# Performance work log

Hardware: AMD Instinct MI355X
Metric: run time of the kernel (lower is better)

Reference implementation:

```python
import jax, jax.numpy as jnp
from jax import lax
import numpy as np

K = 32        # self.k: neighbors queried per center
TOP = 5       # inner topk size (hardcoded in source)
MAX_ITER = 16 # bound on the data-dependent while loop; leftovers emitted at final iter


def _refine_one(pc, centers, ids):
    """Vectorized translation of the per-batch while-loop.

    Instead of shrinking the sample set each iteration (data-dependent shape),
    every sample is tracked with an `active` flag and a convergence-iteration
    stamp. Emitting order in the torch code is (iteration, surviving-order),
    and boolean masking preserves relative original order, so a stable sort by
    (conv_iter, original_index) reproduces the exact concatenation order.
    """
    N, D = pc.shape
    S = centers.shape[0]
    ar = jnp.arange(S)

    def knn(q):  # q: [S,3] -> [S,K] indices of nearest cloud points (ascending dist)
        d2 = jnp.sum((q[:, None, :] - pc[None, :, :]) ** 2, axis=-1)  # [S,N]
        _, ind = lax.top_k(-d2, K)
        return ind

    def step(cur_pts, cur_idx):
        ind = knn(cur_pts)                                   # [S,K]
        nbh = pc[ind]                                        # [S,K,3]
        gc = jnp.mean(nbh, axis=1)                           # [S,3]
        dist = jnp.linalg.norm(nbh - gc[:, None, :], axis=2) # [S,K]
        _, top = lax.top_k(-dist, TOP)                       # [S,TOP] smallest dists
        in_top = jnp.any(top == 0, axis=1)                   # center (col 0) stable?
        new_idx = ind[ar, top[:, 0]]                         # point closest to centroid
        return ind, in_top, new_idx

    def body(it, st):
        cur_pts, cur_idx, conv_it, out_pts, out_idx, out_grp, active = st
        ind, in_top, new_idx = step(cur_pts, cur_idx)
        newly = active & in_top
        conv_it = jnp.where(newly, it, conv_it)
        out_pts = jnp.where(newly[:, None], cur_pts, out_pts)
        out_idx = jnp.where(newly, cur_idx, out_idx)
        out_grp = jnp.where(newly[:, None], ind, out_grp)
        move = active & ~in_top
        cur_idx = jnp.where(move, new_idx, cur_idx)
        cur_pts = jnp.where(move[:, None], pc[new_idx], cur_pts)
        return (cur_pts, cur_idx, conv_it, out_pts, out_idx, out_grp, move)

    st0 = (centers, ids,
           jnp.full((S,), MAX_ITER, jnp.int32),
           jnp.zeros((S, D), pc.dtype),
           jnp.zeros((S,), ids.dtype),
           jnp.zeros((S, K), jnp.int32),
           jnp.ones((S,), bool))
    cur_pts, cur_idx, conv_it, out_pts, out_idx, out_grp, active = lax.fori_loop(
        0, MAX_ITER, body, st0)

    # force-emit any sample that never converged within MAX_ITER
    ind, _, _ = step(cur_pts, cur_idx)
    out_pts = jnp.where(active[:, None], cur_pts, out_pts)
    out_idx = jnp.where(active, cur_idx, out_idx)
    out_grp = jnp.where(active[:, None], ind, out_grp)

    order = jnp.argsort(conv_it * (S + 1) + ar)  # stable (iter, orig-pos) order
    return out_pts[order], out_idx[order], out_grp[order]


def setup_inputs() -> dict:
    key = jax.random.key(0)
    k1, k2, k3 = jax.random.split(key, 3)
    B, N, S = 8, 8192, 1024
    xyz = jax.random.normal(k1, (B, N, 3), jnp.float32)
    center = jax.random.normal(k2, (B, S, 3), jnp.float32)
    idx = jax.random.randint(k3, (B, S), 0, N, jnp.int32)
    return {"xyz": xyz, "center": center, "idx": idx}


def reference(xyz, center, idx):
    assert xyz.shape[0] == center.shape[0]
    C, I1, I2 = jax.vmap(_refine_one)(xyz, center, idx)
    # torch runs under no_grad; outputs are detached constants
    return (lax.stop_gradient(C), I1, I2)
```

## Files before the change

### kernel.cpp

```cpp
#include <hip/hip_runtime.h>
#include <stdint.h>

#define BATCH   8
#define NPTS    8192
#define SCH     1024
#define KNN     32
#define TOPC    5
#define MAXIT   16
#define NCELL   4096
#define NGRP    128
#define NSEED   6
#define FCAP    128

typedef unsigned long long ull;
typedef float vf2 __attribute__((ext_vector_type(2)));
typedef float vf4 __attribute__((ext_vector_type(4)));

#define SENTKEY ((((ull)0x7F800000u) << 13) | 0x1FFFull)

#define ROTL(lane, g) (((lane) + (g) * 17) & 63)

__device__ __forceinline__ uint32_t xshfl32(uint32_t v, int xl) {
    if (xl == 1)
        return (uint32_t)__builtin_amdgcn_update_dpp((int)v, (int)v, 0xB1, 0xF, 0xF, true);
    if (xl == 2)
        return (uint32_t)__builtin_amdgcn_update_dpp((int)v, (int)v, 0x4E, 0xF, 0xF, true);
    return (uint32_t)__shfl_xor((int)v, xl, 64);
}
__device__ __forceinline__ ull xshfl64(ull v, int xl) {
    uint32_t lo = xshfl32((uint32_t)v, xl);
    uint32_t hi = xshfl32((uint32_t)(v >> 32), xl);
    return ((ull)hi << 32) | lo;
}
__device__ __forceinline__ float xshflf(float v, int xl) {
    return __uint_as_float(xshfl32(__float_as_uint(v), xl));
}

__device__ __forceinline__ float d2_exact(vf4 q, vf4 p) {
#pragma clang fp contract(off)
    vf2 d = q.xy - p.xy;
    vf2 s = d * d;
    float dz = q.z - p.z;
    float sz = dz * dz;
    return (s.x + s.y) + sz;
}

__device__ __forceinline__ void insert_top4(ull key, ull& k0, ull& k1, ull& k2,
                                            ull& k3, float& th) {
    if (key < k3) {
        k3 = key;
        { bool c = k3 < k2; ull mn = c ? k3 : k2, mx = c ? k2 : k3; k2 = mn; k3 = mx; }
        { bool c = k2 < k1; ull mn = c ? k2 : k1, mx = c ? k1 : k2; k1 = mn; k2 = mx; }
        { bool c = k1 < k0; ull mn = c ? k1 : k0, mx = c ? k0 : k1; k0 = mn; k1 = mx; }
        th = __uint_as_float((uint32_t)(k3 >> 13));
    }
}

__device__ __forceinline__ ull wave_min_u64(ull k) {
#pragma unroll
    for (int off = 32; off; off >>= 1) {
        ull o = xshfl64(k, off);
        k = o < k ? o : k;
    }
    return k;
}
__device__ __forceinline__ ull wave_max_u64(ull k) {
#pragma unroll
    for (int off = 32; off; off >>= 1) {
        ull o = xshfl64(k, off);
        k = o > k ? o : k;
    }
    return k;
}

__device__ __forceinline__ float bbox_mind2(vf4 q, vf4 c, vf4 h) {
    float dx = fmaxf(fabsf(q.x - c.x) - h.x, 0.f);
    float dy = fmaxf(fabsf(q.y - c.y) - h.y, 0.f);
    float dz = fmaxf(fabsf(q.z - c.z) - h.z, 0.f);
    return (dx * dx + dy * dy + dz * dz) * 0.9999f;
}

__device__ __forceinline__ ull cx(ull v, int xl, bool keepmin) {
    ull o = xshfl64(v, xl);
    return ((v < o) == keepmin) ? v : o;
}
__device__ __forceinline__ void cswap(ull& a, ull& b, bool up) {
    bool lt = a < b;
    ull mn = lt ? a : b, mx = lt ? b : a;
    a = up ? mn : mx;
    b = up ? mx : mn;
}

__device__ __forceinline__ uint32_t cx32(uint32_t v, int xl, bool keepmin) {
    uint32_t o = xshfl32(v, xl);
    return ((v < o) == keepmin) ? v : o;
}
__device__ __forceinline__ void cswap32(uint32_t& a, uint32_t& b, bool up) {
    uint32_t mn = a < b ? a : b, mx = a < b ? b : a;
    a = up ? mn : mx;
    b = up ? mx : mn;
}

__device__ __forceinline__ void sort128_u32(uint32_t& s0, uint32_t& s1, int lane) {
    cswap32(s0, s1, true);
    if (lane & 1) { uint32_t t = s0; s0 = s1; s1 = t; }
#pragma unroll
    for (int kk = 4; kk <= 128; kk <<= 1) {
        const bool up = (lane & (kk >> 1)) == 0;
#pragma unroll
        for (int d = kk >> 1; d >= 2; d >>= 1) {
            const int xl = d >> 1;
            const bool keepmin = (up == ((lane & xl) == 0));
            s0 = cx32(s0, xl, keepmin);
            s1 = cx32(s1, xl, keepmin);
        }
        cswap32(s0, s1, up);
    }
}

__device__ __forceinline__ void sort128_u64(ull& s0, ull& s1, int lane) {
    cswap(s0, s1, true);
    if (lane & 1) { ull t = s0; s0 = s1; s1 = t; }
#pragma unroll
    for (int kk = 4; kk <= 128; kk <<= 1) {
        const bool up = (lane & (kk >> 1)) == 0;
#pragma unroll
        for (int d = kk >> 1; d >= 2; d >>= 1) {
            const int xl = d >> 1;
            const bool keepmin = (up == ((lane & xl) == 0));
            s0 = cx(s0, xl, keepmin);
            s1 = cx(s1, xl, keepmin);
        }
        cswap(s0, s1, up);
    }
}

__device__ __forceinline__ int next_gid(ull& r0, ull& r1) {
    if (r0) { int g = __ffsll((unsigned long long)r0) - 1; r0 &= r0 - 1; return g; }
    if (r1) { int g = __ffsll((unsigned long long)r1) - 1; r1 &= r1 - 1; return 64 + g; }
    return -1;
}

__device__ __forceinline__ int cell_of(float x, float y, float z) {
    int cxi = min(15, max(0, (int)floorf((x + 4.0f) * 2.0f)));
    int cyi = min(15, max(0, (int)floorf((y + 4.0f) * 2.0f)));
    int czi = min(15, max(0, (int)floorf((z + 4.0f) * 2.0f)));
    uint32_t sx = (cxi & 1) | ((cxi & 2) << 2) | ((cxi & 4) << 4) | ((cxi & 8) << 6);
    uint32_t sy = (cyi & 1) | ((cyi & 2) << 2) | ((cyi & 4) << 4) | ((cyi & 8) << 6);
    uint32_t sz = (czi & 1) | ((czi & 2) << 2) | ((czi & 4) << 4) | ((czi & 8) << 6);
    return (int)(sx | (sy << 1) | (sz << 2));
}

__device__ __attribute__((noinline)) int serial_topk_masked(
    const vf4* __restrict__ Psort, vf4 q, int lane, ull sm0, ull sm1) {
    ull k0 = SENTKEY, k1 = SENTKEY, k2 = SENTKEY, k3 = SENTKEY;
    int s0 = 0, s1 = 0, s2 = 0, s3 = 0;
    float th = __builtin_inff();
    for (int gid = 0; gid < NGRP; ++gid) {
        bool sel = (gid < 64) ? ((sm0 >> gid) & 1ull) : ((sm1 >> (gid - 64)) & 1ull);
        if (!sel) continue;
        vf4 p = Psort[(gid << 6) + lane];
        float d2 = d2_exact(q, p);
        uint32_t oi = __float_as_uint(p.w);
        ull key = ((ull)__float_as_uint(d2) << 13) | oi;
        if (d2 <= th && key < k3) {
            k3 = key; s3 = gid;
            if (k3 < k2) { ull t = k2; k2 = k3; k3 = t; int ts = s2; s2 = s3; s3 = ts; }
            if (k2 < k1) { ull t = k1; k1 = k2; k2 = t; int ts = s1; s1 = s2; s2 = ts; }
            if (k1 < k0) { ull t = k0; k0 = k1; k1 = t; int ts = s0; s0 = s1; s1 = ts; }
            th = __uint_as_float((uint32_t)(k3 >> 13));
        }
    }
    ull em0 = 0ull, em1 = 0ull;
    int cnt = 4, my_ind = 0;
    for (int r = 0; r < KNN; ++r) {
        ull gmin = wave_min_u64(k0);
        int widx = (int)(gmin & 0x1FFFull);
        if (lane == r) my_ind = widx;
        if (k0 == gmin) {
            int g = s0;
            if (g < 64) em0 |= 1ull << g; else em1 |= 1ull << (g - 64);
            k0 = k1; k1 = k2; k2 = k3; k3 = SENTKEY;
            s0 = s1; s1 = s2; s2 = s3;
            if (--cnt == 0) {
                k0 = k1 = k2 = k3 = SENTKEY;
                float th2 = __builtin_inff();
                for (int gid = 0; gid < NGRP; ++gid) {
                    bool sel = (gid < 64) ? ((sm0 >> gid) & 1ull)
                                          : ((sm1 >> (gid - 64)) & 1ull);
                    bool ex = (gid < 64) ? ((em0 >> gid) & 1ull)
                                         : ((em1 >> (gid - 64)) & 1ull);
                    if (!sel || ex) continue;
                    vf4 p = Psort[(gid << 6) + lane];
                    float d2 = d2_exact(q, p);
                    uint32_t oi = __float_as_uint(p.w);
                    ull key = ((ull)__float_as_uint(d2) << 13) | oi;
                    if (d2 <= th2 && key < k3) {
                        k3 = key; s3 = gid;
                        if (k3 < k2) { ull t = k2; k2 = k3; k3 = t; int ts = s2; s2 = s3; s3 = ts; }
                        if (k2 < k1) { ull t = k1; k1 = k2; k2 = t; int ts = s1; s1 = s2; s2 = ts; }
                        if (k1 < k0) { ull t = k0; k0 = k1; k1 = t; int ts = s0; s0 = s1; s1 = ts; }
                        th2 = __uint_as_float((uint32_t)(k3 >> 13));
                    }
                }
                cnt = 4;
            }
        }
    }
    return my_ind;
}

__device__ int collect_topk(const vf4* __restrict__ Psort, vf4 q, int lane,
                            ull sm0, ull sm1, ull tau,
                            ull* buf, int* cnt) {
    if (lane == 0) *cnt = 0;
    __asm__ volatile("s_waitcnt lgkmcnt(0)" ::: "memory");
    ull r0 = sm0, r1 = sm1;
    int g = next_gid(r0, r1);
    while (g >= 0) {
        vf4 p = Psort[(g << 6) + lane];
        float d2 = d2_exact(q, p);
        ull key = ((ull)__float_as_uint(d2) << 13) | __float_as_uint(p.w);
        if (key <= tau) {
            int pos = atomicAdd(cnt, 1);
            if (pos < FCAP) buf[pos] = key;
        }
        g = next_gid(r0, r1);
    }
    __asm__ volatile("s_waitcnt lgkmcnt(0)" ::: "memory");
    const int M = *cnt;
    if (M > FCAP) return -1;
    ull s0 = (2 * lane + 0 < M) ? buf[2 * lane + 0] : SENTKEY;
    ull s1 = (2 * lane + 1 < M) ? buf[2 * lane + 1] : SENTKEY;
    sort128_u64(s0, s1, lane);
    const int src = lane >> 1;
    const uint32_t e0 = (uint32_t)__shfl((int)(uint32_t)s0, src, 64);
    const uint32_t e1 = (uint32_t)__shfl((int)(uint32_t)s1, src, 64);
    return (int)(((lane & 1) ? e1 : e0) & 0x1FFFu);
}

__global__ __launch_bounds__(256) void prep_kernel(const float* __restrict__ xyz,
                                                   vf4* __restrict__ pc4,
                                                   int* __restrict__ counts) {
    int i = (int)(blockIdx.x * blockDim.x + threadIdx.x);
    if (i >= BATCH * NPTS) return;
    vf4 v;
    v.x = xyz[(size_t)i * 3 + 0];
    v.y = xyz[(size_t)i * 3 + 1];
    v.z = xyz[(size_t)i * 3 + 2];
    v.w = 0.f;
    pc4[i] = v;
    int b = i >> 13;
    atomicAdd(&counts[b * NCELL + cell_of(v.x, v.y, v.z)], 1);
}

__global__ __launch_bounds__(1024) void scan_kernel(const int* __restrict__ counts,
                                                    int* __restrict__ cursor) {
    int b = (int)blockIdx.x, tid = (int)threadIdx.x;
    int lane = tid & 63, w = tid >> 6;
    __shared__ int wsum[16];
    int base = b * NCELL + tid * 4;
    int v0 = counts[base], v1 = counts[base + 1], v2 = counts[base + 2], v3 = counts[base + 3];
    int s = v0 + v1 + v2 + v3;
    int incl = s;
#pragma unroll
    for (int off = 1; off < 64; off <<= 1) {
        int o = __shfl_up(incl, off, 64);
        if (lane >= off) incl += o;
    }
    if (lane == 63) wsum[w] = incl;
    __syncthreads();
    if (tid == 0) {
        int acc = 0;
#pragma unroll
        for (int i = 0; i < 16; ++i) { int x = wsum[i]; wsum[i] = acc; acc += x; }
    }
    __syncthreads();
    int excl = incl - s + wsum[w];
    cursor[base]     = excl;
    cursor[base + 1] = excl + v0;
    cursor[base + 2] = excl + v0 + v1;
    cursor[base + 3] = excl + v0 + v1 + v2;
}

__global__ __launch_bounds__(256) void scatter_kernel(const vf4* __restrict__ pc4,
                                                      int* __restrict__ cursor,
                                                      vf4* __restrict__ sortedP) {
    int i = (int)(blockIdx.x * blockDim.x + threadIdx.x);
    if (i >= BATCH * NPTS) return;
    vf4 v = pc4[i];
    int b = i >> 13, pi = i & (NPTS - 1);
    int c = cell_of(v.x, v.y, v.z);
    int pos = atomicAdd(&cursor[b * NCELL + c], 1);
    v.w = __uint_as_float((uint32_t)pi);
    sortedP[((size_t)b << 13) + pos] = v;
}

__global__ __launch_bounds__(256) void bbox_kernel(const vf4* __restrict__ sortedP,
                                                   vf4* __restrict__ bC,
                                                   vf4* __restrict__ bH) {
    int g = (int)((blockIdx.x * blockDim.x + threadIdx.x) >> 6);
    int lane = (int)(threadIdx.x & 63);
    vf4 p = sortedP[((size_t)g << 6) + lane];
    float mnx = p.x, mxx = p.x, mny = p.y, mxy = p.y, mnz = p.z, mxz = p.z;
#pragma unroll
    for (int off = 32; off; off >>= 1) {
        mnx = fminf(mnx, xshflf(mnx, off));
        mxx = fmaxf(mxx, xshflf(mxx, off));
        mny = fminf(mny, xshflf(mny, off));
        mxy = fmaxf(mxy, xshflf(mxy, off));
        mnz = fminf(mnz, xshflf(mnz, off));
        mxz = fmaxf(mxz, xshflf(mxz, off));
    }
    if (lane == 0) {
        vf4 c, h;
        c.x = (mnx + mxx) * 0.5f; c.y = (mny + mxy) * 0.5f; c.z = (mnz + mxz) * 0.5f; c.w = 0.f;
        h.x = (mxx - mnx) * 0.5f; h.y = (mxy - mny) * 0.5f; h.z = (mxz - mnz) * 0.5f; h.w = 0.f;
        bC[g] = c;
        bH[g] = h;
    }
}

__global__ __launch_bounds__(256)
__attribute__((amdgpu_waves_per_eu(2, 4)))
void refine_kernel(
    const vf4* __restrict__ pc4, const vf4* __restrict__ sortedP,
    const vf4* __restrict__ bC, const vf4* __restrict__ bH,
    const float* __restrict__ center, const int* __restrict__ idx_in,
    float* __restrict__ pts_ws, int* __restrict__ idx_ws,
    int* __restrict__ grp_ws, int* __restrict__ conv_ws) {
    const int lane = (int)(threadIdx.x & 63);
    const int w = (int)(threadIdx.x >> 6);
    const int b = (int)(blockIdx.x & 7);
    const int s = (((int)blockIdx.x >> 3) << 2) + w;
    const vf4* __restrict__ Porig = pc4 + ((size_t)b << 13);
    const vf4* __restrict__ Psort = sortedP + ((size_t)b << 13);

    __shared__ vf4 sbC[NGRP], sbH[NGRP];
    __shared__ vf4 nbh[4][KNN];
    __shared__ ull fbuf[4][FCAP];
    __shared__ int fcnt[4];

    {
        const int t = (int)threadIdx.x;
        if (t < NGRP) sbC[t] = bC[(b << 7) + t];
        else          sbH[t - NGRP] = bH[(b << 7) + (t - NGRP)];
    }
    __syncthreads();

    const size_t ch = ((size_t)b << 10) + (size_t)s;
    vf4 q;
    q.x = center[ch * 3 + 0];
    q.y = center[ch * 3 + 1];
    q.z = center[ch * 3 + 2];
    q.w = 0.f;
    int qidx = idx_in[ch];

    int conv = MAXIT;
    int my_ind = 0;
    vf4 myp = q;
    bool warm = false;

    for (int it = 0;; ++it) {
        const vf4 c0 = sbC[lane],      h0 = sbH[lane];
        const vf4 c1 = sbC[64 + lane], h1 = sbH[64 + lane];
        const float m0 = bbox_mind2(q, c0, h0);
        const float m1 = bbox_mind2(q, c1, h1);

        ull k0 = SENTKEY, k1 = SENTKEY, k2 = SENTKEY, k3 = SENTKEY;
        float th = __builtin_inff();
        ull sm0 = 0ull, sm1 = 0ull, am0 = 0ull, am1 = 0ull;
        float th0 = __builtin_inff();

        bool fastwarm = false;
        if (warm) {
            const float dw = (lane < KNN) ? d2_exact(q, myp) : 0.f;
            th0 = dw;
#pragma unroll
            for (int off = 32; off; off >>= 1)
                th0 = fmaxf(th0, xshflf(th0, off));
            sm0 = __ballot(m0 <= th0);
            sm1 = __ballot(m1 <= th0);
            const int nsel = __popcll(sm0) + __popcll(sm1);
            if (nsel <= 20) { fastwarm = true; am0 = sm0; am1 = sm1; }
        }

        if (!fastwarm) {
            sm0 = 0ull; sm1 = 0ull;
            uint32_t g0k = ((__float_as_uint(m0) >> 6) << 7) | (uint32_t)lane;
            uint32_t g1k = ((__float_as_uint(m1) >> 6) << 7) | (uint32_t)(64 + lane);
            sort128_u32(g0k, g1k, lane);
#pragma unroll
            for (int r = 0; r < NSEED; ++r) {
                const uint32_t nk = (r & 1)
                    ? (uint32_t)__shfl((int)g1k, r >> 1, 64)
                    : (uint32_t)__shfl((int)g0k, r >> 1, 64);
                const int gid = (int)(nk & 127u);
                if (gid < 64) sm0 |= 1ull << gid; else sm1 |= 1ull << (gid - 64);
                const vf4 p = Psort[(gid << 6) + ROTL(lane, gid)];
                const float d2 = d2_exact(q, p);
                if (d2 <= th)
                    insert_top4(((ull)__float_as_uint(d2) << 13) | __float_as_uint(p.w),
                                k0, k1, k2, k3, th);
            }
            ull t = k0;
            {
                ull o = xshfl64(t, 32);
                t = o < t ? o : t;
            }
            const ull B = wave_max_u64(t);
            const float Bd = fminf(__uint_as_float((uint32_t)(B >> 13)), th0);
            am0 = __ballot(m0 <= Bd) & ~sm0;
            am1 = __ballot(m1 <= Bd) & ~sm1;
            sm0 |= am0; sm1 |= am1;
        }

        {
            ull rem0 = am0, rem1 = am1;
            int ga = next_gid(rem0, rem1);
            while (ga >= 0) {
                const int gb2 = next_gid(rem0, rem1);
                const vf4 pa = Psort[(ga << 6) + ROTL(lane, ga)];
                vf4 pb;
                if (gb2 >= 0) pb = Psort[(gb2 << 6) + ROTL(lane, gb2)];
                const float da = d2_exact(q, pa);
                if (da <= th)
                    insert_top4(((ull)__float_as_uint(da) << 13) | __float_as_uint(pa.w),
                                k0, k1, k2, k3, th);
                if (gb2 >= 0) {
                    const float dbv = d2_exact(q, pb);
                    if (dbv <= th)
                        insert_top4(((ull)__float_as_uint(dbv) << 13) | __float_as_uint(pb.w),
                                    k0, k1, k2, k3, th);
                }
                ga = next_gid(rem0, rem1);
            }
        }
        const ull prek3 = k3;

        const bool odd = (lane & 1) != 0;
        ull a0 = odd ? k3 : k0;
        ull a1 = odd ? k2 : k1;
        ull a2 = odd ? k1 : k2;
        ull a3 = odd ? k0 : k3;
#pragma unroll
        for (int kk = 8; kk <= 256; kk <<= 1) {
            const bool up = (lane & (kk >> 2)) == 0;
#pragma unroll
            for (int d = kk >> 1; d >= 4; d >>= 1) {
                const int xl = d >> 2;
                const bool keepmin = (up == ((lane & xl) == 0));
                a0 = cx(a0, xl, keepmin);
                a1 = cx(a1, xl, keepmin);
                a2 = cx(a2, xl, keepmin);
                a3 = cx(a3, xl, keepmin);
            }
            cswap(a0, a2, up); cswap(a1, a3, up);
            cswap(a0, a1, up); cswap(a2, a3, up);
        }
        const ull tau = (ull)__shfl((unsigned long long)a3, 7, 64);
        const ull bad = __ballot(prek3 < tau);
        if (bad != 0ull) {
            const int mi = collect_topk(Psort, q, lane, sm0, sm1, tau,
                                        fbuf[w], &fcnt[w]);
            my_ind = (mi >= 0) ? mi : serial_topk_masked(Psort, q, lane, sm0, sm1);
        } else {
            const int src = lane >> 2;
            const uint32_t lo0 = (uint32_t)__shfl((int)(uint32_t)a0, src, 64);
            const uint32_t lo1 = (uint32_t)__shfl((int)(uint32_t)a1, src, 64);
            const uint32_t lo2 = (uint32_t)__shfl((int)(uint32_t)a2, src, 64);
            const uint32_t lo3 = (uint32_t)__shfl((int)(uint32_t)a3, src, 64);
            const int sel = lane & 3;
            uint32_t lo = (sel == 0) ? lo0 : (sel == 1) ? lo1 : (sel == 2) ? lo2 : lo3;
            my_ind = (int)(lo & 0x1FFFu);
        }

        if (it == MAXIT) break;

        myp = q;
        if (lane < KNN) {
            myp = Porig[my_ind];
            nbh[w][lane] = myp;
        }
        __asm__ volatile("s_waitcnt lgkmcnt(0)" ::: "memory");
        float sx = 0.f, sy = 0.f, sz = 0.f;
#pragma unroll
        for (int j = 0; j < KNN; ++j) {
            vf4 pj = nbh[w][j];
            sx = __fadd_rn(sx, pj.x);
            sy = __fadd_rn(sy, pj.y);
            sz = __fadd_rn(sz, pj.z);
        }
        const float gx = __fmul_rn(sx, 0.03125f);
        const float gy = __fmul_rn(sy, 0.03125f);
        const float gz = __fmul_rn(sz, 0.03125f);

        float dj = __builtin_inff();
        if (lane < KNN) {
            const float dx = __fsub_rn(myp.x, gx);
            const float dy = __fsub_rn(myp.y, gy);
            const float dz = __fsub_rn(myp.z, gz);
            dj = sqrtf(__fadd_rn(__fadd_rn(__fmul_rn(dx, dx), __fmul_rn(dy, dy)),
                                 __fmul_rn(dz, dz)));
        }
        const uint32_t db = __float_as_uint(dj);
        const uint32_t d0 = (uint32_t)__shfl((int)db, 0, 64);
        const ull bal = __ballot(db < d0);
        if (__popcll(bal) <= TOPC - 1) { conv = it; break; }

        uint32_t m = db;
#pragma unroll
        for (int off = 32; off; off >>= 1) {
            uint32_t o = xshfl32(m, off);
            m = o < m ? o : m;
        }
        const ull balm = __ballot(db == m);
        const int jm = __ffsll((unsigned long long)balm) - 1;
        qidx = __shfl(my_ind, jm, 64);
        q.x = __shfl(myp.x, jm, 64);
        q.y = __shfl(myp.y, jm, 64);
        q.z = __shfl(myp.z, jm, 64);
        q.w = 0.f;
        warm = true;
    }

    if (lane < KNN) grp_ws[ch * KNN + lane] = my_ind;
    if (lane == 0) {
        pts_ws[ch * 3 + 0] = q.x;
        pts_ws[ch * 3 + 1] = q.y;
        pts_ws[ch * 3 + 2] = q.z;
        idx_ws[ch] = qidx;
        conv_ws[ch] = conv;
    }
}

__global__ __launch_bounds__(1024) void order_kernel(
    const float* __restrict__ pts_ws, const int* __restrict__ idx_ws,
    const int* __restrict__ grp_ws, const int* __restrict__ conv_ws,
    float* __restrict__ out) {
    const int b = (int)blockIdx.x;
    const int s = (int)threadIdx.x;
    const int w = s >> 6, l = s & 63;
    __shared__ int wavecnt[16][MAXIT + 1];
    __shared__ int binbase[MAXIT + 1];
    const size_t ch = (size_t)b * SCH + s;
    const int c = conv_ws[ch];
    int rw = 0;
#pragma unroll
    for (int v = 0; v <= MAXIT; ++v) {
        ull bal = __ballot(c == v);
        if (l == 0) wavecnt[w][v] = (int)__popcll(bal);
        if (c == v) rw = (int)__popcll(bal & ((1ull << l) - 1ull));
    }
    __syncthreads();
    if (s == 0) {
        int acc = 0;
        for (int v = 0; v <= MAXIT; ++v) {
            int t = 0;
            for (int w2 = 0; w2 < 16; ++w2) t += wavecnt[w2][v];
            binbase[v] = acc;
            acc += t;
        }
    }
    __syncthreads();
    int pos = binbase[c] + rw;
    for (int w2 = 0; w2 < w; ++w2) pos += wavecnt[w2][c];

    float* __restrict__ C  = out;
    float* __restrict__ I1 = out + (size_t)BATCH * SCH * 3;
    float* __restrict__ I2 = I1 + (size_t)BATCH * SCH;
    const size_t o = (size_t)b * SCH + pos;
    C[o * 3 + 0] = pts_ws[ch * 3 + 0];
    C[o * 3 + 1] = pts_ws[ch * 3 + 1];
    C[o * 3 + 2] = pts_ws[ch * 3 + 2];
    I1[o] = (float)idx_ws[ch];
#pragma unroll
    for (int k = 0; k < KNN; ++k) I2[o * KNN + k] = (float)grp_ws[ch * KNN + k];
}

extern "C" void kernel_launch(void* const* d_in, const int* in_sizes, int n_in,
                              void* d_out, int out_size, void* d_ws, size_t ws_size,
                              hipStream_t stream) {
    const float* xyz    = (const float*)d_in[0];
    const float* center = (const float*)d_in[1];
    const int*   idx_in = (const int*)d_in[2];
    float* out = (float*)d_out;

    char* wp = (char*)d_ws;
    vf4* pc4     = (vf4*)wp;  wp += (size_t)BATCH * NPTS * sizeof(vf4);
    vf4* sortedP = (vf4*)wp;  wp += (size_t)BATCH * NPTS * sizeof(vf4);
    vf4* bC      = (vf4*)wp;  wp += (size_t)BATCH * NGRP * sizeof(vf4);
    vf4* bH      = (vf4*)wp;  wp += (size_t)BATCH * NGRP * sizeof(vf4);
    int* counts  = (int*)wp;  wp += (size_t)BATCH * NCELL * 4;
    int* cursor  = (int*)wp;  wp += (size_t)BATCH * NCELL * 4;
    float* pts_ws = (float*)wp; wp += (size_t)BATCH * SCH * 3 * 4;
    int*   idx_ws = (int*)wp;   wp += (size_t)BATCH * SCH * 4;
    int*   grp_ws = (int*)wp;   wp += (size_t)BATCH * SCH * KNN * 4;
    int*   conv_ws = (int*)wp;

    hipMemsetAsync(counts, 0, (size_t)BATCH * NCELL * 4, stream);
    prep_kernel<<<(BATCH * NPTS + 255) / 256, 256, 0, stream>>>(xyz, pc4, counts);
    scan_kernel<<<BATCH, 1024, 0, stream>>>(counts, cursor);
    scatter_kernel<<<(BATCH * NPTS + 255) / 256, 256, 0, stream>>>(pc4, cursor, sortedP);
    bbox_kernel<<<(BATCH * NGRP * 64) / 256, 256, 0, stream>>>(sortedP, bC, bH);

    const int chains = BATCH * SCH;
    refine_kernel<<<chains * 64 / 256, 256, 0, stream>>>(
        pc4, sortedP, bC, bH, center, idx_in, pts_ws, idx_ws, grp_ws, conv_ws);
    order_kernel<<<BATCH, SCH, 0, stream>>>(pts_ws, idx_ws, grp_ws, conv_ws, out);
}
```

Baseline: 180.8 us.

## Fuse bbox computation into scatter via atomics and ordering into refine tail

Removes the separate bbox kernel by computing per-group min/max bounds with order-preserving float-encoded atomicMin/Max inside the scatter kernel. Also removes the order kernel: the last refine block per batch, found through an atomic done counter, computes the convergence-order permutation with shared bitmasks and writes the outputs. This saves two launches but adds many contended global atomics in scatter and serialises the ordering work onto a single tail block per batch with 256 threads.

```diff
diff --git a/kernel.cpp b/kernel.cpp
--- a/kernel.cpp
+++ b/kernel.cpp
@@ -20,6 +20,15 @@
 
 #define ROTL(lane, g) (((lane) + (g) * 17) & 63)
 
+__device__ __forceinline__ uint32_t fenc(float f) {
+    uint32_t b = __float_as_uint(f);
+    return (b & 0x80000000u) ? ~b : (b | 0x80000000u);
+}
+__device__ __forceinline__ float fdec(uint32_t u) {
+    uint32_t b = (u & 0x80000000u) ? (u & 0x7FFFFFFFu) : ~u;
+    return __uint_as_float(b);
+}
+
 __device__ __forceinline__ uint32_t xshfl32(uint32_t v, int xl) {
     if (xl == 1)
         return (uint32_t)__builtin_amdgcn_update_dpp((int)v, (int)v, 0xB1, 0xF, 0xF, true);
@@ -73,10 +82,10 @@
     return k;
 }
 
-__device__ __forceinline__ float bbox_mind2(vf4 q, vf4 c, vf4 h) {
-    float dx = fmaxf(fabsf(q.x - c.x) - h.x, 0.f);
-    float dy = fmaxf(fabsf(q.y - c.y) - h.y, 0.f);
-    float dz = fmaxf(fabsf(q.z - c.z) - h.z, 0.f);
+__device__ __forceinline__ float bbox_mind2_mm(vf4 q, vf4 mn, vf4 mx) {
+    float dx = fmaxf(fmaxf(mn.x - q.x, q.x - mx.x), 0.f);
+    float dy = fmaxf(fmaxf(mn.y - q.y, q.y - mx.y), 0.f);
+    float dz = fmaxf(fmaxf(mn.z - q.z, q.z - mx.z), 0.f);
     return (dx * dx + dy * dy + dz * dz) * 0.9999f;
 }
 
@@ -241,9 +250,12 @@
 
 __global__ __launch_bounds__(256) void prep_kernel(const float* __restrict__ xyz,
                                                    vf4* __restrict__ pc4,
-                                                   int* __restrict__ counts) {
+                                                   int* __restrict__ counts,
+                                                   uint32_t* __restrict__ bMinU,
+                                                   uint32_t* __restrict__ bMaxU) {
     int i = (int)(blockIdx.x * blockDim.x + threadIdx.x);
     if (i >= BATCH * NPTS) return;
+    if (i < BATCH * NGRP * 3) { bMinU[i] = 0xFFFFFFFFu; bMaxU[i] = 0u; }
     vf4 v;
     v.x = xyz[(size_t)i * 3 + 0];
     v.y = xyz[(size_t)i * 3 + 1];
@@ -285,50 +297,35 @@
 
 __global__ __launch_bounds__(256) void scatter_kernel(const vf4* __restrict__ pc4,
                                                       int* __restrict__ cursor,
-                                                      vf4* __restrict__ sortedP) {
+                                                      vf4* __restrict__ sortedP,
+                                                      uint32_t* __restrict__ bMinU,
+                                                      uint32_t* __restrict__ bMaxU) {
     int i = (int)(blockIdx.x * blockDim.x + threadIdx.x);
     if (i >= BATCH * NPTS) return;
     vf4 v = pc4[i];
     int b = i >> 13, pi = i & (NPTS - 1);
     int c = cell_of(v.x, v.y, v.z);
     int pos = atomicAdd(&cursor[b * NCELL + c], 1);
+    const int g = ((b << 7) + (pos >> 6)) * 3;
+    atomicMin(&bMinU[g + 0], fenc(v.x));
+    atomicMin(&bMinU[g + 1], fenc(v.y));
+    atomicMin(&bMinU[g + 2], fenc(v.z));
+    atomicMax(&bMaxU[g + 0], fenc(v.x));
+    atomicMax(&bMaxU[g + 1], fenc(v.y));
+    atomicMax(&bMaxU[g + 2], fenc(v.z));
     v.w = __uint_as_float((uint32_t)pi);
     sortedP[((size_t)b << 13) + pos] = v;
-}
-
-__global__ __launch_bounds__(256) void bbox_kernel(const vf4* __restrict__ sortedP,
-                                                   vf4* __restrict__ bC,
-                                                   vf4* __restrict__ bH) {
-    int g = (int)((blockIdx.x * blockDim.x + threadIdx.x) >> 6);
-    int lane = (int)(threadIdx.x & 63);
-    vf4 p = sortedP[((size_t)g << 6) + lane];
-    float mnx = p.x, mxx = p.x, mny = p.y, mxy = p.y, mnz = p.z, mxz = p.z;
-#pragma unroll
-    for (int off = 32; off; off >>= 1) {
-        mnx = fminf(mnx, xshflf(mnx, off));
-        mxx = fmaxf(mxx, xshflf(mxx, off));
-        mny = fminf(mny, xshflf(mny, off));
-        mxy = fmaxf(mxy, xshflf(mxy, off));
-        mnz = fminf(mnz, xshflf(mnz, off));
-        mxz = fmaxf(mxz, xshflf(mxz, off));
-    }
-    if (lane == 0) {
-        vf4 c, h;
-        c.x = (mnx + mxx) * 0.5f; c.y = (mny + mxy) * 0.5f; c.z = (mnz + mxz) * 0.5f; c.w = 0.f;
-        h.x = (mxx - mnx) * 0.5f; h.y = (mxy - mny) * 0.5f; h.z = (mxz - mnz) * 0.5f; h.w = 0.f;
-        bC[g] = c;
-        bH[g] = h;
-    }
 }
 
 __global__ __launch_bounds__(256)
 __attribute__((amdgpu_waves_per_eu(2, 4)))
 void refine_kernel(
     const vf4* __restrict__ pc4, const vf4* __restrict__ sortedP,
-    const vf4* __restrict__ bC, const vf4* __restrict__ bH,
+    const uint32_t* __restrict__ bMinU, const uint32_t* __restrict__ bMaxU,
     const float* __restrict__ center, const int* __restrict__ idx_in,
     float* __restrict__ pts_ws, int* __restrict__ idx_ws,
-    int* __restrict__ grp_ws, int* __restrict__ conv_ws) {
+    int* __restrict__ grp_ws, int* __restrict__ conv_ws,
+    float* __restrict__ out, int* __restrict__ done) {
     const int lane = (int)(threadIdx.x & 63);
     const int w = (int)(threadIdx.x >> 6);
     const int b = (int)(blockIdx.x & 7);
@@ -336,15 +333,30 @@
     const vf4* __restrict__ Porig = pc4 + ((size_t)b << 13);
     const vf4* __restrict__ Psort = sortedP + ((size_t)b << 13);
 
-    __shared__ vf4 sbC[NGRP], sbH[NGRP];
+    __shared__ vf4 sMn[NGRP], sMx[NGRP];
     __shared__ vf4 nbh[4][KNN];
     __shared__ ull fbuf[4][FCAP];
     __shared__ int fcnt[4];
+    __shared__ ull binmask[MAXIT + 1][16];
+    __shared__ int binbase2[MAXIT + 1];
+    __shared__ int lastflag;
 
     {
         const int t = (int)threadIdx.x;
-        if (t < NGRP) sbC[t] = bC[(b << 7) + t];
-        else          sbH[t - NGRP] = bH[(b << 7) + (t - NGRP)];
+        if (t < NGRP) {
+            const int gi = ((b << 7) + t) * 3;
+            vf4 v;
+            v.x = fdec(bMinU[gi + 0]); v.y = fdec(bMinU[gi + 1]);
+            v.z = fdec(bMinU[gi + 2]); v.w = 0.f;
+            sMn[t] = v;
+        } else {
+            const int tt = t - NGRP;
+            const int gi = ((b << 7) + tt) * 3;
+            vf4 v;
+            v.x = fdec(bMaxU[gi + 0]); v.y = fdec(bMaxU[gi + 1]);
+            v.z = fdec(bMaxU[gi + 2]); v.w = 0.f;
+            sMx[tt] = v;
+        }
     }
     __syncthreads();
 
@@ -362,10 +374,8 @@
     bool warm = false;
 
     for (int it = 0;; ++it) {
-        const vf4 c0 = sbC[lane],      h0 = sbH[lane];
-        const vf4 c1 = sbC[64 + lane], h1 = sbH[64 + lane];
-        const float m0 = bbox_mind2(q, c0, h0);
-        const float m1 = bbox_mind2(q, c1, h1);
+        const float m0 = bbox_mind2_mm(q, sMn[lane], sMx[lane]);
+        const float m1 = bbox_mind2_mm(q, sMn[64 + lane], sMx[64 + lane]);
 
         ull k0 = SENTKEY, k1 = SENTKEY, k2 = SENTKEY, k3 = SENTKEY;
         float th = __builtin_inff();
@@ -532,50 +542,60 @@
         idx_ws[ch] = qidx;
         conv_ws[ch] = conv;
     }
-}
-
-__global__ __launch_bounds__(1024) void order_kernel(
-    const float* __restrict__ pts_ws, const int* __restrict__ idx_ws,
-    const int* __restrict__ grp_ws, const int* __restrict__ conv_ws,
-    float* __restrict__ out) {
-    const int b = (int)blockIdx.x;
-    const int s = (int)threadIdx.x;
-    const int w = s >> 6, l = s & 63;
-    __shared__ int wavecnt[16][MAXIT + 1];
-    __shared__ int binbase[MAXIT + 1];
-    const size_t ch = (size_t)b * SCH + s;
-    const int c = conv_ws[ch];
-    int rw = 0;
-#pragma unroll
-    for (int v = 0; v <= MAXIT; ++v) {
-        ull bal = __ballot(c == v);
-        if (l == 0) wavecnt[w][v] = (int)__popcll(bal);
-        if (c == v) rw = (int)__popcll(bal & ((1ull << l) - 1ull));
-    }
-    __syncthreads();
-    if (s == 0) {
+
+    __syncthreads();
+    if (threadIdx.x == 0) {
+        __threadfence();
+        const int prev = atomicAdd(&done[b], 1);
+        lastflag = (prev == (SCH / 4) - 1);
+    }
+    __syncthreads();
+    if (!lastflag) return;
+    __threadfence();
+
+    const int t = (int)threadIdx.x;
+    for (int i = t; i < (MAXIT + 1) * 16; i += 256)
+        ((ull*)binmask)[i] = 0ull;
+    __syncthreads();
+    int cvals[4];
+#pragma unroll
+    for (int pass = 0; pass < 4; ++pass) {
+        const int s2 = pass * 256 + t;
+        const int c = conv_ws[((size_t)b << 10) + s2];
+        cvals[pass] = c;
+        atomicOr(&binmask[c][s2 >> 6], 1ull << (s2 & 63));
+    }
+    __syncthreads();
+    if (t == 0) {
         int acc = 0;
         for (int v = 0; v <= MAXIT; ++v) {
-            int t = 0;
-            for (int w2 = 0; w2 < 16; ++w2) t += wavecnt[w2][v];
-            binbase[v] = acc;
-            acc += t;
-        }
-    }
-    __syncthreads();
-    int pos = binbase[c] + rw;
-    for (int w2 = 0; w2 < w; ++w2) pos += wavecnt[w2][c];
-
+            int cnt2 = 0;
+            for (int w2 = 0; w2 < 16; ++w2) cnt2 += (int)__popcll(binmask[v][w2]);
+            binbase2[v] = acc;
+            acc += cnt2;
+        }
+    }
+    __syncthreads();
     float* __restrict__ C  = out;
     float* __restrict__ I1 = out + (size_t)BATCH * SCH * 3;
     float* __restrict__ I2 = I1 + (size_t)BATCH * SCH;
-    const size_t o = (size_t)b * SCH + pos;
-    C[o * 3 + 0] = pts_ws[ch * 3 + 0];
-    C[o * 3 + 1] = pts_ws[ch * 3 + 1];
-    C[o * 3 + 2] = pts_ws[ch * 3 + 2];
-    I1[o] = (float)idx_ws[ch];
-#pragma unroll
-    for (int k = 0; k < KNN; ++k) I2[o * KNN + k] = (float)grp_ws[ch * KNN + k];
+#pragma unroll
+    for (int pass = 0; pass < 4; ++pass) {
+        const int s2 = pass * 256 + t;
+        const int c = cvals[pass];
+        int r = 0;
+        for (int w2 = 0; w2 < (s2 >> 6); ++w2) r += (int)__popcll(binmask[c][w2]);
+        r += (int)__popcll(binmask[c][s2 >> 6] & ((1ull << (s2 & 63)) - 1ull));
+        const int pos = binbase2[c] + r;
+        const size_t chs = ((size_t)b << 10) + s2;
+        const size_t o = ((size_t)b << 10) + pos;
+        C[o * 3 + 0] = pts_ws[chs * 3 + 0];
+        C[o * 3 + 1] = pts_ws[chs * 3 + 1];
+        C[o * 3 + 2] = pts_ws[chs * 3 + 2];
+        I1[o] = (float)idx_ws[chs];
+        for (int k = 0; k < KNN; ++k)
+            I2[o * KNN + k] = (float)grp_ws[chs * KNN + k];
+    }
 }
 
 extern "C" void kernel_launch(void* const* d_in, const int* in_sizes, int n_in,
@@ -589,23 +609,25 @@
     char* wp = (char*)d_ws;
     vf4* pc4     = (vf4*)wp;  wp += (size_t)BATCH * NPTS * sizeof(vf4);
     vf4* sortedP = (vf4*)wp;  wp += (size_t)BATCH * NPTS * sizeof(vf4);
-    vf4* bC      = (vf4*)wp;  wp += (size_t)BATCH * NGRP * sizeof(vf4);
-    vf4* bH      = (vf4*)wp;  wp += (size_t)BATCH * NGRP * sizeof(vf4);
+    uint32_t* bMinU = (uint32_t*)wp; wp += (size_t)BATCH * NGRP * 3 * 4;
+    uint32_t* bMaxU = (uint32_t*)wp; wp += (size_t)BATCH * NGRP * 3 * 4;
     int* counts  = (int*)wp;  wp += (size_t)BATCH * NCELL * 4;
+    int* done    = (int*)wp;  wp += 32;
     int* cursor  = (int*)wp;  wp += (size_t)BATCH * NCELL * 4;
     float* pts_ws = (float*)wp; wp += (size_t)BATCH * SCH * 3 * 4;
     int*   idx_ws = (int*)wp;   wp += (size_t)BATCH * SCH * 4;
     int*   grp_ws = (int*)wp;   wp += (size_t)BATCH * SCH * KNN * 4;
     int*   conv_ws = (int*)wp;
 
-    hipMemsetAsync(counts, 0, (size_t)BATCH * NCELL * 4, stream);
-    prep_kernel<<<(BATCH * NPTS + 255) / 256, 256, 0, stream>>>(xyz, pc4, counts);
+    hipMemsetAsync(counts, 0, (size_t)BATCH * NCELL * 4 + 32, stream);
+    prep_kernel<<<(BATCH * NPTS + 255) / 256, 256, 0, stream>>>(
+        xyz, pc4, counts, bMinU, bMaxU);
     scan_kernel<<<BATCH, 1024, 0, stream>>>(counts, cursor);
-    scatter_kernel<<<(BATCH * NPTS + 255) / 256, 256, 0, stream>>>(pc4, cursor, sortedP);
-    bbox_kernel<<<(BATCH * NGRP * 64) / 256, 256, 0, stream>>>(sortedP, bC, bH);
+    scatter_kernel<<<(BATCH * NPTS + 255) / 256, 256, 0, stream>>>(
+        pc4, cursor, sortedP, bMinU, bMaxU);
 
     const int chains = BATCH * SCH;
     refine_kernel<<<chains * 64 / 256, 256, 0, stream>>>(
-        pc4, sortedP, bC, bH, center, idx_in, pts_ws, idx_ws, grp_ws, conv_ws);
-    order_kernel<<<BATCH, SCH, 0, stream>>>(pts_ws, idx_ws, grp_ws, conv_ws, out);
-}
+        pc4, sortedP, bMinU, bMaxU, center, idx_in,
+        pts_ws, idx_ws, grp_ws, conv_ws, out, done);
+}
```

After: 238.4 us. +31.8%, slower.
